# Optimization experiments

Hardware: AMD Instinct MI355X
Metric: run time of the kernel (lower is better)

Reference implementation:

```python
import jax, jax.numpy as jnp
import numpy as np

B, N, E = 256, 4096, 65536  # graphs, nodes/graph (64*64), edges/graph


def setup_inputs() -> dict:
    key = jax.random.key(0)
    k = jax.random.split(key, 6)
    x = jax.random.normal(k[0], (B, N, 3), dtype=jnp.float32)
    src = jax.random.randint(k[1], (E,), 0, N, dtype=jnp.int32)
    dst = jax.random.randint(k[2], (E,), 0, N, dtype=jnp.int32)
    W1 = jax.random.normal(k[3], (3, 64), dtype=jnp.float32) * 0.3
    b1 = jnp.zeros((64,), dtype=jnp.float32)
    Wfc = jax.random.normal(k[4], (N * 64, 1), dtype=jnp.float32) * 0.002
    bfc = jnp.zeros((1,), dtype=jnp.float32)
    return {"x": x, "W1": W1, "b1": b1, "Wfc": Wfc, "bfc": bfc,
            "src": src, "dst": dst}


def reference(x, W1, b1, Wfc, bfc, src, dst):
    # DGL GraphConv, norm='both': h = relu(D_in^{-1/2} A D_out^{-1/2} x W + b)
    ones = jnp.ones((E,), dtype=x.dtype)
    deg_out = jax.ops.segment_sum(ones, src, num_segments=N)
    deg_in = jax.ops.segment_sum(ones, dst, num_segments=N)
    c_src = jax.lax.rsqrt(jnp.maximum(deg_out, 1.0))  # [N]
    c_dst = jax.lax.rsqrt(jnp.maximum(deg_in, 1.0))   # [N]
    # gather normalized source features, scatter-add into destinations
    msg = (x * c_src[None, :, None])[:, src]          # [B, E, 3]
    agg = jnp.zeros_like(x).at[:, dst].add(msg)       # [B, N, 3]
    h = jax.nn.relu((agg * c_dst[None, :, None]) @ W1 + b1)  # [B, N, 64]
    # fc: flatten per graph, Linear(N*64 -> 1) + sigmoid
    logits = h.reshape(x.shape[0], -1) @ Wfc + bfc    # [B, 1]
    return jax.nn.sigmoid(logits)
```

## Files before the change

kernel.cpp:

```cpp
#include <hip/hip_runtime.h>
#include <math.h>

#define Bg 256
#define Nn 4096
#define Ee 65536
#define Kk (Nn * 3)

__device__ __forceinline__ unsigned bf16r(float v) {
    unsigned b = __float_as_uint(v);
    return (b + 0x7fffu + ((b >> 16) & 1u)) >> 16;
}

__global__ __launch_bounds__(256) void k_prep(const int* __restrict__ src,
                                              const int* __restrict__ dst,
                                              int* __restrict__ deg_out,
                                              int* __restrict__ cursor,
                                              int* __restrict__ csr) {
    int e = blockIdx.x * 256 + threadIdx.x;
    if (e < Ee) {
        int s = src[e], d = dst[e];
        atomicAdd(&deg_out[s], 1);
        int ofs = atomicAdd(&cursor[d], 1) & 63;
        csr[(d << 6) + ofs] = s;
    }
}

__global__ __launch_bounds__(256) void k_transpose(const float* __restrict__ x,
                                                   const int* __restrict__ deg_out,
                                                   uint2* __restrict__ xsb) {
    __shared__ float4 tile4[64][49];
    __shared__ float cs[64];
    int t = threadIdx.x;
    int n0 = blockIdx.x * 64;
    int bq = blockIdx.y;
    if (t < 64) cs[t] = rsqrtf(fmaxf((float)deg_out[n0 + t], 1.0f));
    const float* xb = x + (size_t)bq * 64 * Kk + (size_t)n0 * 3;
#pragma unroll
    for (int i = 0; i < 12; i++) {
        int idx = i * 256 + t;
        int bi = idx / 48, j = idx - bi * 48;
        tile4[bi][j] = ((const float4*)(xb + (size_t)bi * Kk))[j];
    }
    __syncthreads();
    const float* tile = (const float*)tile4;
    uint2* outp = xsb + ((size_t)bq * Nn + n0) * 64;
#pragma unroll
    for (int i = 0; i < 16; i++) {
        int idx = i * 256 + t;
        int nn = idx >> 6, bl = idx & 63;
        float c = cs[nn];
        float f0 = tile[bl * 196 + nn * 3 + 0] * c;
        float f1 = tile[bl * 196 + nn * 3 + 1] * c;
        float f2 = tile[bl * 196 + nn * 3 + 2] * c;
        uint2 u;
        u.x = bf16r(f0) | (bf16r(f1) << 16);
        u.y = bf16r(f2);
        outp[(size_t)nn * 64 + bl] = u;
    }
}

__global__ __launch_bounds__(256) void k_main(const uint2* __restrict__ xsb,
                                              const float* __restrict__ W1,
                                              const float* __restrict__ b1,
                                              const float* __restrict__ Wfc,
                                              const int* __restrict__ cursor,
                                              const int* __restrict__ csr,
                                              float* __restrict__ partial) {
    __shared__ float4 sW14[64];
    __shared__ float sWfc[4][64];
    __shared__ float red[4][64];
    int t = threadIdx.x & 63;
    int w = threadIdx.x >> 6;
    int bq = blockIdx.x & 3;
    int g  = blockIdx.x >> 2;
    int n  = g * 4 + w;
    if (w == 0) sW14[t] = make_float4(W1[t], W1[64 + t], W1[128 + t], b1[t]);
    sWfc[w][t] = Wfc[n * 64 + t];
    __syncthreads();

    const uint2* slab = xsb + (size_t)bq * (Nn * 64);
    const int* row = csr + (n << 6);
    int deg = cursor[n]; if (deg > 64) deg = 64;
    float a0 = 0.f, a1 = 0.f, a2 = 0.f;
    float c0 = 0.f, c1 = 0.f, c2 = 0.f;
    int i = 0;
    for (; i + 8 <= deg; i += 8) {
        uint2 u0 = slab[(row[i + 0] << 6) + t];
        uint2 u1 = slab[(row[i + 1] << 6) + t];
        uint2 u2 = slab[(row[i + 2] << 6) + t];
        uint2 u3 = slab[(row[i + 3] << 6) + t];
        uint2 u4 = slab[(row[i + 4] << 6) + t];
        uint2 u5 = slab[(row[i + 5] << 6) + t];
        uint2 u6 = slab[(row[i + 6] << 6) + t];
        uint2 u7 = slab[(row[i + 7] << 6) + t];
        a0 += __uint_as_float(u0.x << 16); a1 += __uint_as_float(u0.x & 0xffff0000u); a2 += __uint_as_float(u0.y << 16);
        c0 += __uint_as_float(u1.x << 16); c1 += __uint_as_float(u1.x & 0xffff0000u); c2 += __uint_as_float(u1.y << 16);
        a0 += __uint_as_float(u2.x << 16); a1 += __uint_as_float(u2.x & 0xffff0000u); a2 += __uint_as_float(u2.y << 16);
        c0 += __uint_as_float(u3.x << 16); c1 += __uint_as_float(u3.x & 0xffff0000u); c2 += __uint_as_float(u3.y << 16);
        a0 += __uint_as_float(u4.x << 16); a1 += __uint_as_float(u4.x & 0xffff0000u); a2 += __uint_as_float(u4.y << 16);
        c0 += __uint_as_float(u5.x << 16); c1 += __uint_as_float(u5.x & 0xffff0000u); c2 += __uint_as_float(u5.y << 16);
        a0 += __uint_as_float(u6.x << 16); a1 += __uint_as_float(u6.x & 0xffff0000u); a2 += __uint_as_float(u6.y << 16);
        c0 += __uint_as_float(u7.x << 16); c1 += __uint_as_float(u7.x & 0xffff0000u); c2 += __uint_as_float(u7.y << 16);
    }
    for (; i < deg; i++) {
        uint2 u = slab[(row[i] << 6) + t];
        a0 += __uint_as_float(u.x << 16);
        a1 += __uint_as_float(u.x & 0xffff0000u);
        a2 += __uint_as_float(u.y << 16);
    }
    a0 += c0; a1 += c1; a2 += c2;
    float cd = rsqrtf(fmaxf((float)deg, 1.0f));
    a0 *= cd; a1 *= cd; a2 *= cd;

    float part = 0.f;
#pragma unroll 8
    for (int f = 0; f < 64; f++) {
        float4 wv = sW14[f];
        float h = fmaf(a0, wv.x, fmaf(a1, wv.y, fmaf(a2, wv.z, wv.w)));
        part = fmaf(fmaxf(h, 0.f), sWfc[w][f], part);
    }
    red[w][t] = part;
    __syncthreads();
    if (w == 0) {
        float tot = (red[0][t] + red[1][t]) + (red[2][t] + red[3][t]);
        partial[(size_t)g * 256 + bq * 64 + t] = tot;
    }
}

__global__ __launch_bounds__(256) void k_reduce(const float* __restrict__ partial,
                                                float* __restrict__ out_acc) {
    int t = threadIdx.x;
    int g0 = blockIdx.x * 16;
    float s = 0.f;
#pragma unroll
    for (int g = 0; g < 16; g++) s += partial[(size_t)(g0 + g) * 256 + t];
    atomicAdd(&out_acc[t], s);
}

__global__ __launch_bounds__(256) void k_final(const float* __restrict__ out_acc,
                                               const float* __restrict__ bfc,
                                               float* __restrict__ out) {
    int t = threadIdx.x;
    float v = out_acc[t] + bfc[0];
    out[t] = 1.0f / (1.0f + expf(-v));
}

extern "C" void kernel_launch(void* const* d_in, const int* in_sizes, int n_in,
                              void* d_out, int out_size, void* d_ws, size_t ws_size,
                              hipStream_t stream) {
    const float* x   = (const float*)d_in[0];
    const float* W1  = (const float*)d_in[1];
    const float* b1  = (const float*)d_in[2];
    const float* Wfc = (const float*)d_in[3];
    const float* bfc = (const float*)d_in[4];
    const int*   src = (const int*)d_in[5];
    const int*   dst = (const int*)d_in[6];
    float* out = (float*)d_out;

    char* ws = (char*)d_ws;
    uint2* xsb = (uint2*)ws;
    const size_t Z = (size_t)4 * Nn * 64 * 8;
    int*   deg_out = (int*)(ws + Z);
    int*   cursor  = (int*)(ws + Z + 16384);
    float* out_acc = (float*)(ws + Z + 32768);
    int*   csr     = (int*)(ws + Z + 33792);
    float* partial = (float*)(ws + Z + 33792 + 1048576);

    hipMemsetAsync(ws + Z, 0, 33792, stream);
    k_prep<<<Ee / 256, 256, 0, stream>>>(src, dst, deg_out, cursor, csr);
    k_transpose<<<dim3(Nn / 64, 4), 256, 0, stream>>>(x, deg_out, xsb);
    k_main<<<1024 * 4, 256, 0, stream>>>(xsb, W1, b1, Wfc, cursor, csr, partial);
    k_reduce<<<64, 256, 0, stream>>>(partial, out_acc);
    k_final<<<1, 256, 0, stream>>>(out_acc, bfc, out);
}
```

Baseline: 109.2 us.

## Fuse prep with transpose, apply source norm in gather, fuse reduce with sigmoid

Runs the edge-degree/CSR build and the x transpose as two roles of one launch. This removes the dependency on deg_out from the transpose by applying the source-degree rsqrt per edge inside the gather loop. Reduce and final sigmoid merge into one kernel, where a ticket counter lets the last block finish. The transposed bf16 slab is also written twice (8 copies instead of 4) so alternating node groups read different copies. The aim is fewer launches and serialization points, paid for with extra deg_out loads and rsqrt per edge and double the transpose write traffic.

Result: slower. 113.4 us (+3.9%).

```diff
diff --git a/kernel.cpp b/kernel.cpp
--- a/kernel.cpp
+++ b/kernel.cpp
@@ -11,13 +11,45 @@
     return (b + 0x7fffu + ((b >> 16) & 1u)) >> 16;
 }
 
-__global__ __launch_bounds__(256) void k_prep(const int* __restrict__ src,
-                                              const int* __restrict__ dst,
-                                              int* __restrict__ deg_out,
-                                              int* __restrict__ cursor,
-                                              int* __restrict__ csr) {
-    int e = blockIdx.x * 256 + threadIdx.x;
-    if (e < Ee) {
+__global__ __launch_bounds__(256) void k_prep_transpose(const float* __restrict__ x,
+                                                        const int* __restrict__ src,
+                                                        const int* __restrict__ dst,
+                                                        int* __restrict__ deg_out,
+                                                        int* __restrict__ cursor,
+                                                        int* __restrict__ csr,
+                                                        uint2* __restrict__ xsb) {
+    int id = blockIdx.x;
+    int t = threadIdx.x;
+    if (id < 512) {
+        __shared__ float4 tile4[64][49];
+        int k = id & 7;
+        int g = id >> 3;
+        int n0 = g * 64;
+        int b0 = (k & 3) * 64;
+        const float* xb = x + (size_t)b0 * Kk + (size_t)n0 * 3;
+#pragma unroll
+        for (int i = 0; i < 12; i++) {
+            int idx = i * 256 + t;
+            int bi = idx / 48, j = idx - bi * 48;
+            tile4[bi][j] = ((const float4*)(xb + (size_t)bi * Kk))[j];
+        }
+        __syncthreads();
+        const float* tile = (const float*)tile4;
+        uint2* outp = xsb + ((size_t)k * Nn + n0) * 64;
+#pragma unroll
+        for (int i = 0; i < 16; i++) {
+            int idx = i * 256 + t;
+            int nn = idx >> 6, bl = idx & 63;
+            float f0 = tile[bl * 196 + nn * 3 + 0];
+            float f1 = tile[bl * 196 + nn * 3 + 1];
+            float f2 = tile[bl * 196 + nn * 3 + 2];
+            uint2 u;
+            u.x = bf16r(f0) | (bf16r(f1) << 16);
+            u.y = bf16r(f2);
+            outp[(size_t)nn * 64 + bl] = u;
+        }
+    } else {
+        int e = (id - 512) * 256 + t;
         int s = src[e], d = dst[e];
         atomicAdd(&deg_out[s], 1);
         int ofs = atomicAdd(&cursor[d], 1) & 63;
@@ -25,44 +57,11 @@
     }
 }
 
-__global__ __launch_bounds__(256) void k_transpose(const float* __restrict__ x,
-                                                   const int* __restrict__ deg_out,
-                                                   uint2* __restrict__ xsb) {
-    __shared__ float4 tile4[64][49];
-    __shared__ float cs[64];
-    int t = threadIdx.x;
-    int n0 = blockIdx.x * 64;
-    int bq = blockIdx.y;
-    if (t < 64) cs[t] = rsqrtf(fmaxf((float)deg_out[n0 + t], 1.0f));
-    const float* xb = x + (size_t)bq * 64 * Kk + (size_t)n0 * 3;
-#pragma unroll
-    for (int i = 0; i < 12; i++) {
-        int idx = i * 256 + t;
-        int bi = idx / 48, j = idx - bi * 48;
-        tile4[bi][j] = ((const float4*)(xb + (size_t)bi * Kk))[j];
-    }
-    __syncthreads();
-    const float* tile = (const float*)tile4;
-    uint2* outp = xsb + ((size_t)bq * Nn + n0) * 64;
-#pragma unroll
-    for (int i = 0; i < 16; i++) {
-        int idx = i * 256 + t;
-        int nn = idx >> 6, bl = idx & 63;
-        float c = cs[nn];
-        float f0 = tile[bl * 196 + nn * 3 + 0] * c;
-        float f1 = tile[bl * 196 + nn * 3 + 1] * c;
-        float f2 = tile[bl * 196 + nn * 3 + 2] * c;
-        uint2 u;
-        u.x = bf16r(f0) | (bf16r(f1) << 16);
-        u.y = bf16r(f2);
-        outp[(size_t)nn * 64 + bl] = u;
-    }
-}
-
 __global__ __launch_bounds__(256) void k_main(const uint2* __restrict__ xsb,
                                               const float* __restrict__ W1,
                                               const float* __restrict__ b1,
                                               const float* __restrict__ Wfc,
+                                              const int* __restrict__ deg_out,
                                               const int* __restrict__ cursor,
                                               const int* __restrict__ csr,
                                               float* __restrict__ partial) {
@@ -71,6 +70,7 @@
     __shared__ float red[4][64];
     int t = threadIdx.x & 63;
     int w = threadIdx.x >> 6;
+    int sq = blockIdx.x & 7;
     int bq = blockIdx.x & 3;
     int g  = blockIdx.x >> 2;
     int n  = g * 4 + w;
@@ -78,38 +78,46 @@
     sWfc[w][t] = Wfc[n * 64 + t];
     __syncthreads();
 
-    const uint2* slab = xsb + (size_t)bq * (Nn * 64);
+    const uint2* slab = xsb + (size_t)sq * (Nn * 64);
     const int* row = csr + (n << 6);
-    int deg = cursor[n]; if (deg > 64) deg = 64;
+    int degv = cursor[n];
+    int deg = degv > 64 ? 64 : degv;
     float a0 = 0.f, a1 = 0.f, a2 = 0.f;
-    float c0 = 0.f, c1 = 0.f, c2 = 0.f;
+    float e0 = 0.f, e1 = 0.f, e2 = 0.f;
     int i = 0;
-    for (; i + 8 <= deg; i += 8) {
-        uint2 u0 = slab[(row[i + 0] << 6) + t];
-        uint2 u1 = slab[(row[i + 1] << 6) + t];
-        uint2 u2 = slab[(row[i + 2] << 6) + t];
-        uint2 u3 = slab[(row[i + 3] << 6) + t];
-        uint2 u4 = slab[(row[i + 4] << 6) + t];
-        uint2 u5 = slab[(row[i + 5] << 6) + t];
-        uint2 u6 = slab[(row[i + 6] << 6) + t];
-        uint2 u7 = slab[(row[i + 7] << 6) + t];
-        a0 += __uint_as_float(u0.x << 16); a1 += __uint_as_float(u0.x & 0xffff0000u); a2 += __uint_as_float(u0.y << 16);
-        c0 += __uint_as_float(u1.x << 16); c1 += __uint_as_float(u1.x & 0xffff0000u); c2 += __uint_as_float(u1.y << 16);
-        a0 += __uint_as_float(u2.x << 16); a1 += __uint_as_float(u2.x & 0xffff0000u); a2 += __uint_as_float(u2.y << 16);
-        c0 += __uint_as_float(u3.x << 16); c1 += __uint_as_float(u3.x & 0xffff0000u); c2 += __uint_as_float(u3.y << 16);
-        a0 += __uint_as_float(u4.x << 16); a1 += __uint_as_float(u4.x & 0xffff0000u); a2 += __uint_as_float(u4.y << 16);
-        c0 += __uint_as_float(u5.x << 16); c1 += __uint_as_float(u5.x & 0xffff0000u); c2 += __uint_as_float(u5.y << 16);
-        a0 += __uint_as_float(u6.x << 16); a1 += __uint_as_float(u6.x & 0xffff0000u); a2 += __uint_as_float(u6.y << 16);
-        c0 += __uint_as_float(u7.x << 16); c1 += __uint_as_float(u7.x & 0xffff0000u); c2 += __uint_as_float(u7.y << 16);
+    for (; i + 4 <= deg; i += 4) {
+        int s0 = row[i], s1 = row[i + 1], s2 = row[i + 2], s3 = row[i + 3];
+        float q0 = rsqrtf(fmaxf((float)deg_out[s0], 1.f));
+        float q1 = rsqrtf(fmaxf((float)deg_out[s1], 1.f));
+        float q2 = rsqrtf(fmaxf((float)deg_out[s2], 1.f));
+        float q3 = rsqrtf(fmaxf((float)deg_out[s3], 1.f));
+        uint2 u0 = slab[(s0 << 6) + t];
+        uint2 u1 = slab[(s1 << 6) + t];
+        uint2 u2 = slab[(s2 << 6) + t];
+        uint2 u3 = slab[(s3 << 6) + t];
+        a0 = fmaf(__uint_as_float(u0.x << 16), q0, a0);
+        a1 = fmaf(__uint_as_float(u0.x & 0xffff0000u), q0, a1);
+        a2 = fmaf(__uint_as_float(u0.y << 16), q0, a2);
+        e0 = fmaf(__uint_as_float(u1.x << 16), q1, e0);
+        e1 = fmaf(__uint_as_float(u1.x & 0xffff0000u), q1, e1);
+        e2 = fmaf(__uint_as_float(u1.y << 16), q1, e2);
+        a0 = fmaf(__uint_as_float(u2.x << 16), q2, a0);
+        a1 = fmaf(__uint_as_float(u2.x & 0xffff0000u), q2, a1);
+        a2 = fmaf(__uint_as_float(u2.y << 16), q2, a2);
+        e0 = fmaf(__uint_as_float(u3.x << 16), q3, e0);
+        e1 = fmaf(__uint_as_float(u3.x & 0xffff0000u), q3, e1);
+        e2 = fmaf(__uint_as_float(u3.y << 16), q3, e2);
     }
     for (; i < deg; i++) {
-        uint2 u = slab[(row[i] << 6) + t];
-        a0 += __uint_as_float(u.x << 16);
-        a1 += __uint_as_float(u.x & 0xffff0000u);
-        a2 += __uint_as_float(u.y << 16);
+        int s = row[i];
+        float q = rsqrtf(fmaxf((float)deg_out[s], 1.f));
+        uint2 u = slab[(s << 6) + t];
+        a0 = fmaf(__uint_as_float(u.x << 16), q, a0);
+        a1 = fmaf(__uint_as_float(u.x & 0xffff0000u), q, a1);
+        a2 = fmaf(__uint_as_float(u.y << 16), q, a2);
     }
-    a0 += c0; a1 += c1; a2 += c2;
-    float cd = rsqrtf(fmaxf((float)deg, 1.0f));
+    a0 += e0; a1 += e1; a2 += e2;
+    float cd = rsqrtf(fmaxf((float)degv, 1.0f));
     a0 *= cd; a1 *= cd; a2 *= cd;
 
     float part = 0.f;
@@ -127,22 +135,26 @@
     }
 }
 
-__global__ __launch_bounds__(256) void k_reduce(const float* __restrict__ partial,
-                                                float* __restrict__ out_acc) {
+__global__ __launch_bounds__(256) void k_reduce_final(const float* __restrict__ partial,
+                                                      float* __restrict__ out_acc,
+                                                      int* __restrict__ ticket,
+                                                      const float* __restrict__ bfc,
+                                                      float* __restrict__ out) {
+    __shared__ int lastflag;
     int t = threadIdx.x;
     int g0 = blockIdx.x * 16;
     float s = 0.f;
 #pragma unroll
     for (int g = 0; g < 16; g++) s += partial[(size_t)(g0 + g) * 256 + t];
     atomicAdd(&out_acc[t], s);
-}
-
-__global__ __launch_bounds__(256) void k_final(const float* __restrict__ out_acc,
-                                               const float* __restrict__ bfc,
-                                               float* __restrict__ out) {
-    int t = threadIdx.x;
-    float v = out_acc[t] + bfc[0];
-    out[t] = 1.0f / (1.0f + expf(-v));
+    __threadfence();
+    __syncthreads();
+    if (t == 0) lastflag = (atomicAdd(ticket, 1) == 63);
+    __syncthreads();
+    if (lastflag) {
+        float v = atomicAdd(&out_acc[t], 0.0f) + bfc[0];
+        out[t] = 1.0f / (1.0f + expf(-v));
+    }
 }
 
 extern "C" void kernel_launch(void* const* d_in, const int* in_sizes, int n_in,
@@ -159,17 +171,16 @@
 
     char* ws = (char*)d_ws;
     uint2* xsb = (uint2*)ws;
-    const size_t Z = (size_t)4 * Nn * 64 * 8;
+    const size_t Z = (size_t)8 * Nn * 64 * 8;
     int*   deg_out = (int*)(ws + Z);
     int*   cursor  = (int*)(ws + Z + 16384);
     float* out_acc = (float*)(ws + Z + 32768);
-    int*   csr     = (int*)(ws + Z + 33792);
-    float* partial = (float*)(ws + Z + 33792 + 1048576);
+    int*   ticket  = (int*)(ws + Z + 33792);
+    int*   csr     = (int*)(ws + Z + 34816);
+    float* partial = (float*)(ws + Z + 34816 + 1048576);
 
-    hipMemsetAsync(ws + Z, 0, 33792, stream);
-    k_prep<<<Ee / 256, 256, 0, stream>>>(src, dst, deg_out, cursor, csr);
-    k_transpose<<<dim3(Nn / 64, 4), 256, 0, stream>>>(x, deg_out, xsb);
-    k_main<<<1024 * 4, 256, 0, stream>>>(xsb, W1, b1, Wfc, cursor, csr, partial);
-    k_reduce<<<64, 256, 0, stream>>>(partial, out_acc);
-    k_final<<<1, 256, 0, stream>>>(out_acc, bfc, out);
+    hipMemsetAsync(ws + Z, 0, 34816, stream);
+    k_prep_transpose<<<512 + Ee / 256, 256, 0, stream>>>(x, src, dst, deg_out, cursor, csr, xsb);
+    k_main<<<1024 * 4, 256, 0, stream>>>(xsb, W1, b1, Wfc, deg_out, cursor, csr, partial);
+    k_reduce_final<<<64, 256, 0, stream>>>(partial, out_acc, ticket, bfc, out);
 }
```

## Replicate transposed feature slabs per XCD and fuse reduce with final sigmoid

Applied to the files above, without the earlier changes.

The transpose kernel now writes eight copies of the bf16 feature slabs instead of four, duplicating each batch quarter. The main kernel picks its copy by blockIdx&7, so blocks scheduled round-robin onto the eight XCDs each read a private copy. The goal is to spread gather traffic and keep each XCD's working set local in cache, at the cost of twice the transpose writes and workspace. Separately, the reduce and final-sigmoid kernels are merged using a last-block ticket counter, which removes one launch.

New measurement: 118.1 us. 8.1% more time.

```diff
diff --git a/kernel.cpp b/kernel.cpp
--- a/kernel.cpp
+++ b/kernel.cpp
@@ -30,11 +30,14 @@
                                                    uint2* __restrict__ xsb) {
     __shared__ float4 tile4[64][49];
     __shared__ float cs[64];
+    int id = blockIdx.x;
     int t = threadIdx.x;
-    int n0 = blockIdx.x * 64;
-    int bq = blockIdx.y;
+    int k = id & 7;
+    int g = id >> 3;
+    int n0 = g * 64;
+    int b0 = (k & 3) * 64;
     if (t < 64) cs[t] = rsqrtf(fmaxf((float)deg_out[n0 + t], 1.0f));
-    const float* xb = x + (size_t)bq * 64 * Kk + (size_t)n0 * 3;
+    const float* xb = x + (size_t)b0 * Kk + (size_t)n0 * 3;
 #pragma unroll
     for (int i = 0; i < 12; i++) {
         int idx = i * 256 + t;
@@ -43,7 +46,7 @@
     }
     __syncthreads();
     const float* tile = (const float*)tile4;
-    uint2* outp = xsb + ((size_t)bq * Nn + n0) * 64;
+    uint2* outp = xsb + ((size_t)k * Nn + n0) * 64;
 #pragma unroll
     for (int i = 0; i < 16; i++) {
         int idx = i * 256 + t;
@@ -71,6 +74,7 @@
     __shared__ float red[4][64];
     int t = threadIdx.x & 63;
     int w = threadIdx.x >> 6;
+    int sq = blockIdx.x & 7;
     int bq = blockIdx.x & 3;
     int g  = blockIdx.x >> 2;
     int n  = g * 4 + w;
@@ -78,7 +82,7 @@
     sWfc[w][t] = Wfc[n * 64 + t];
     __syncthreads();
 
-    const uint2* slab = xsb + (size_t)bq * (Nn * 64);
+    const uint2* slab = xsb + (size_t)sq * (Nn * 64);
     const int* row = csr + (n << 6);
     int deg = cursor[n]; if (deg > 64) deg = 64;
     float a0 = 0.f, a1 = 0.f, a2 = 0.f;
@@ -127,22 +131,26 @@
     }
 }
 
-__global__ __launch_bounds__(256) void k_reduce(const float* __restrict__ partial,
-                                                float* __restrict__ out_acc) {
+__global__ __launch_bounds__(256) void k_reduce_final(const float* __restrict__ partial,
+                                                      float* __restrict__ out_acc,
+                                                      int* __restrict__ ticket,
+                                                      const float* __restrict__ bfc,
+                                                      float* __restrict__ out) {
+    __shared__ int lastflag;
     int t = threadIdx.x;
     int g0 = blockIdx.x * 16;
     float s = 0.f;
 #pragma unroll
     for (int g = 0; g < 16; g++) s += partial[(size_t)(g0 + g) * 256 + t];
     atomicAdd(&out_acc[t], s);
-}
-
-__global__ __launch_bounds__(256) void k_final(const float* __restrict__ out_acc,
-                                               const float* __restrict__ bfc,
-                                               float* __restrict__ out) {
-    int t = threadIdx.x;
-    float v = out_acc[t] + bfc[0];
-    out[t] = 1.0f / (1.0f + expf(-v));
+    __threadfence();
+    __syncthreads();
+    if (t == 0) lastflag = (atomicAdd(ticket, 1) == 63);
+    __syncthreads();
+    if (lastflag) {
+        float v = atomicAdd(&out_acc[t], 0.0f) + bfc[0];
+        out[t] = 1.0f / (1.0f + expf(-v));
+    }
 }
 
 extern "C" void kernel_launch(void* const* d_in, const int* in_sizes, int n_in,
@@ -159,17 +167,17 @@
 
     char* ws = (char*)d_ws;
     uint2* xsb = (uint2*)ws;
-    const size_t Z = (size_t)4 * Nn * 64 * 8;
+    const size_t Z = (size_t)8 * Nn * 64 * 8;
     int*   deg_out = (int*)(ws + Z);
     int*   cursor  = (int*)(ws + Z + 16384);
     float* out_acc = (float*)(ws + Z + 32768);
-    int*   csr     = (int*)(ws + Z + 33792);
-    float* partial = (float*)(ws + Z + 33792 + 1048576);
+    int*   ticket  = (int*)(ws + Z + 33792);
+    int*   csr     = (int*)(ws + Z + 34816);
+    float* partial = (float*)(ws + Z + 34816 + 1048576);
 
-    hipMemsetAsync(ws + Z, 0, 33792, stream);
+    hipMemsetAsync(ws + Z, 0, 34816, stream);
     k_prep<<<Ee / 256, 256, 0, stream>>>(src, dst, deg_out, cursor, csr);
-    k_transpose<<<dim3(Nn / 64, 4), 256, 0, stream>>>(x, deg_out, xsb);
+    k_transpose<<<512, 256, 0, stream>>>(x, deg_out, xsb);
     k_main<<<1024 * 4, 256, 0, stream>>>(xsb, W1, b1, Wfc, cursor, csr, partial);
-    k_reduce<<<64, 256, 0, stream>>>(partial, out_acc);
-    k_final<<<1, 256, 0, stream>>>(out_acc, bfc, out);
+    k_reduce_final<<<64, 256, 0, stream>>>(partial, out_acc, ticket, bfc, out);
 }
```
